# Optimization experiments

Measured on AMD Instinct MI355X. Metric: run time of the kernel, lower is better.

## Reference

```python
import jax, jax.numpy as jnp
import numpy as np

N_BUF = 60000.0
S_INIT = 2.0
S_INV = N_BUF ** S_INIT          # buffer init: N**S_init
S_HAT = (N_BUF ** 2) / S_INV     # == 1.0 at init


def setup_inputs() -> dict:
    key = jax.random.key(0)
    k1, k2 = jax.random.split(key)
    feats = jax.random.normal(k1, (16384, 128), dtype=jnp.float32)
    idx = jax.random.randint(k2, (16384,), 0, 60000).astype(jnp.int64)
    return {"feats": feats, "idx": idx}


def reference(feats, idx):
    # CauchyLoss.forward, faithful to the torch source. Note: the original
    # uses out-of-place masked_fill whose result is discarded, so neither the
    # diagonal nor the positive pairs are zeroed before the row-sum; we
    # replicate that exactly.
    n = feats.shape[0]
    B = n // 2
    sq = jnp.sum(feats * feats, axis=1)                      # [2B]
    d2 = sq[:, None] + sq[None, :] - 2.0 * (feats @ feats.T)  # [2B, 2B]
    d2 = jnp.maximum(d2, 0.0)
    q = 1.0 / (d2 + 1.0)                                      # [2B, 2B]
    # positive pairs: pos_mask = roll(eye(2B), B, dims=1) -> (i, (i+B) % 2B)
    rows = jnp.arange(n)
    qii = q[rows, (rows + B) % n]                             # [2B]
    attractive = -jnp.log(qii)
    repulsive = jnp.log(jnp.sum(q, axis=1)) * S_HAT           # [2B]
    return attractive.mean() + repulsive.mean()
```

## Files before the change

kernel.cpp:

```cpp
#include <hip/hip_runtime.h>
#include <hip/hip_bf16.h>

#define N 16384
#define D 128
#define NTI 128
#define NCHUNK 2112
#define GBLK2 4224
#define B_HALF 8192

typedef __attribute__((ext_vector_type(8))) short short8;
typedef __attribute__((ext_vector_type(4))) float f32x4;

__device__ inline unsigned short f2bf(float x) {
    union { float f; unsigned u; } c; c.f = x;
    unsigned r = c.u + 0x7fffu + ((c.u >> 16) & 1u);
    return (unsigned short)(r >> 16);
}

__global__ __launch_bounds__(256)
void prep_kernel(const float* __restrict__ feats, unsigned short* __restrict__ fbP,
                 float* __restrict__ sq, float* __restrict__ rsum,
                 float* __restrict__ qii) {
    const int g  = blockIdx.x * 256 + threadIdx.x;
    const int p  = g >> 3;
    const int t8 = g & 7;
    const int i0 = p, i1 = p + B_HALF;
    const float4* ra = reinterpret_cast<const float4*>(feats + (size_t)i0 * D + t8 * 16);
    const float4* rb = reinterpret_cast<const float4*>(feats + (size_t)i1 * D + t8 * 16);
    char* da = (char*)fbP + (size_t)(i0 >> 7) * 32768 + (size_t)(i0 & 127) * 16;
    char* db = (char*)fbP + (size_t)(i1 >> 7) * 32768 + (size_t)(i1 & 127) * 16;
    float sa = 0.f, sb = 0.f, dot = 0.f;
#pragma unroll
    for (int c = 0; c < 2; ++c) {
        float4 x0 = ra[2 * c], x1 = ra[2 * c + 1];
        float4 y0 = rb[2 * c], y1 = rb[2 * c + 1];
        sa  += x0.x * x0.x + x0.y * x0.y + x0.z * x0.z + x0.w * x0.w
             + x1.x * x1.x + x1.y * x1.y + x1.z * x1.z + x1.w * x1.w;
        sb  += y0.x * y0.x + y0.y * y0.y + y0.z * y0.z + y0.w * y0.w
             + y1.x * y1.x + y1.y * y1.y + y1.z * y1.z + y1.w * y1.w;
        dot += x0.x * y0.x + x0.y * y0.y + x0.z * y0.z + x0.w * y0.w
             + x1.x * y1.x + x1.y * y1.y + x1.z * y1.z + x1.w * y1.w;
        short8 ca, cb;
        ca[0] = f2bf(x0.x); ca[1] = f2bf(x0.y); ca[2] = f2bf(x0.z); ca[3] = f2bf(x0.w);
        ca[4] = f2bf(x1.x); ca[5] = f2bf(x1.y); ca[6] = f2bf(x1.z); ca[7] = f2bf(x1.w);
        cb[0] = f2bf(y0.x); cb[1] = f2bf(y0.y); cb[2] = f2bf(y0.z); cb[3] = f2bf(y0.w);
        cb[4] = f2bf(y1.x); cb[5] = f2bf(y1.y); cb[6] = f2bf(y1.z); cb[7] = f2bf(y1.w);
        *reinterpret_cast<short8*>(da + (2 * t8 + c) * 2048) = ca;
        *reinterpret_cast<short8*>(db + (2 * t8 + c) * 2048) = cb;
    }
    sa  += __shfl_xor(sa, 1);  sa  += __shfl_xor(sa, 2);  sa  += __shfl_xor(sa, 4);
    sb  += __shfl_xor(sb, 1);  sb  += __shfl_xor(sb, 2);  sb  += __shfl_xor(sb, 4);
    dot += __shfl_xor(dot, 1); dot += __shfl_xor(dot, 2); dot += __shfl_xor(dot, 4);
    if (t8 == 0) {
        sq[i0] = sa; sq[i1] = sb;
        rsum[i0] = 0.f; rsum[i1] = 0.f;
        float d2 = fmaxf(sa + sb - 2.f * dot, 0.f);
        float q = 1.f / (d2 + 1.f);
        qii[i0] = q; qii[i1] = q;
    }
}

__global__ __launch_bounds__(256, 4)
void gram_kernel(const unsigned short* __restrict__ fbP, const float* __restrict__ sq,
                 float* __restrict__ rsum) {
    const int bid  = (blockIdx.x & 7) * (GBLK2 / 8) + (blockIdx.x >> 3);
    const int chnk = bid >> 1;
    const int half = bid & 1;

    int u = (int)((130.0f - sqrtf(16900.0f - 8.0f * (float)chnk)) * 0.25f);
    if (u < 0) u = 0; if (u > 31) u = 31;
    while (u > 0 && 2 * u * (65 - u) > chnk) --u;
    while (2 * (u + 1) * (64 - u) <= chnk) ++u;
    int rem = chnk - 2 * u * (65 - u);
    const int cnt = 32 - u;
    int sub = 0;
    while (rem >= cnt) { rem -= cnt; ++sub; }
    const int ti  = 4 * u + sub;
    const int tj0 = ti + 4 * rem;
    const int nt  = (NTI - tj0 < 4) ? (NTI - tj0) : 4;

    const int tid  = threadIdx.x;
    const int lane = tid & 63;
    const int wid  = tid >> 6;
    const int wr   = wid >> 1;
    const int wc   = wid & 1;
    const int lrow = lane & 15;
    const int lk   = lane >> 4;
    const int row0 = half * 64 + wr * 32;

    const char* pa = (const char*)fbP + (size_t)ti * 32768;
    const int aoff0 = lk * 2048 + (row0 + lrow) * 16;
    const int boff0 = lk * 2048 + (wc * 64 + lrow) * 16;

    float SA[2][4];
#pragma unroll
    for (int m = 0; m < 2; ++m) {
        const float4 v = *reinterpret_cast<const float4*>(
            sq + ti * 128 + row0 + m * 16 + lk * 4);
        SA[m][0] = -0.5f * v.x; SA[m][1] = -0.5f * v.y;
        SA[m][2] = -0.5f * v.z; SA[m][3] = -0.5f * v.w;
    }
    float SB[4][4];
#pragma unroll
    for (int t = 0; t < 4; ++t) {
        const int tt = (tj0 + t < NTI) ? (tj0 + t) : (NTI - 1);
#pragma unroll
        for (int n = 0; n < 4; ++n)
            SB[t][n] = -0.5f * (sq[tt * 128 + wc * 64 + n * 16 + lrow] + 1.0f);
    }

    float racc[2][4];
#pragma unroll
    for (int m = 0; m < 2; ++m)
#pragma unroll
        for (int r = 0; r < 4; ++r) racc[m][r] = 0.f;

#pragma unroll
    for (int t = 0; t < 4; ++t) {
        if (t < nt) {
            const char* pb = (const char*)fbP + (size_t)(tj0 + t) * 32768;

            f32x4 acc[2][4];
#pragma unroll
            for (int m = 0; m < 2; ++m)
#pragma unroll
                for (int n = 0; n < 4; ++n)
#pragma unroll
                    for (int r = 0; r < 4; ++r)
                        acc[m][n][r] = SA[m][r] + SB[t][n];

#pragma unroll
            for (int kk = 0; kk < 4; ++kk) {
                short8 av[2], bv[4];
#pragma unroll
                for (int m = 0; m < 2; ++m)
                    av[m] = *reinterpret_cast<const short8*>(pa + aoff0 + kk * 8192 + m * 256);
#pragma unroll
                for (int n = 0; n < 4; ++n)
                    bv[n] = *reinterpret_cast<const short8*>(pb + boff0 + kk * 8192 + n * 256);
#pragma unroll
                for (int m = 0; m < 2; ++m)
#pragma unroll
                    for (int n = 0; n < 4; ++n)
                        acc[m][n] = __builtin_amdgcn_mfma_f32_16x16x32_bf16(
                            av[m], bv[n], acc[m][n], 0, 0, 0);
            }

            float cloc[4] = {0.f, 0.f, 0.f, 0.f};
#pragma unroll
            for (int m = 0; m < 2; ++m)
#pragma unroll
                for (int n = 0; n < 4; ++n)
#pragma unroll
                    for (int r = 0; r < 4; ++r) {
                        float a = fminf(acc[m][n][r], -0.5f);
                        float q = __builtin_amdgcn_rcpf(a);
                        racc[m][r] += q;
                        cloc[n] += q;
                    }
            if (tj0 + t != ti) {
#pragma unroll
                for (int n = 0; n < 4; ++n) {
                    float v = cloc[n];
                    v += __shfl_xor(v, 16);
                    v += __shfl_xor(v, 32);
                    if (lane < 16)
                        atomicAdd(&rsum[(tj0 + t) * 128 + wc * 64 + n * 16 + lrow],
                                  -0.5f * v);
                }
            }
        }
    }

#pragma unroll
    for (int m = 0; m < 2; ++m)
#pragma unroll
        for (int r = 0; r < 4; ++r) {
            float v = racc[m][r];
            v += __shfl_xor(v, 1);
            v += __shfl_xor(v, 2);
            v += __shfl_xor(v, 4);
            v += __shfl_xor(v, 8);
            if (lrow == 0)
                atomicAdd(&rsum[ti * 128 + row0 + m * 16 + lk * 4 + r], -0.5f * v);
        }
}

__global__ __launch_bounds__(256)
void finish1_kernel(const float* __restrict__ rsum, const float* __restrict__ qii,
                    float* __restrict__ partial) {
    __shared__ float red[4];
    const int i = blockIdx.x * 256 + threadIdx.x;
    float v = __logf(rsum[i]) - __logf(qii[i]);
#pragma unroll
    for (int m = 32; m >= 1; m >>= 1) v += __shfl_xor(v, m);
    if ((threadIdx.x & 63) == 0) red[threadIdx.x >> 6] = v;
    __syncthreads();
    if (threadIdx.x == 0) partial[blockIdx.x] = red[0] + red[1] + red[2] + red[3];
}

__global__ __launch_bounds__(64)
void finish2_kernel(const float* __restrict__ partial, unsigned* __restrict__ out) {
    float v = partial[threadIdx.x];
#pragma unroll
    for (int m = 32; m >= 1; m >>= 1) v += __shfl_xor(v, m);
    if (threadIdx.x == 0) {
        float val = v / (float)N;
        union { float f; unsigned u; } c; c.f = val;
        out[0] = (c.u & 0xFFFF0000u) | (unsigned)f2bf(val);
    }
}

extern "C" void kernel_launch(void* const* d_in, const int* in_sizes, int n_in,
                              void* d_out, int out_size, void* d_ws, size_t ws_size,
                              hipStream_t stream) {
    const float* feats = (const float*)d_in[0];
    char* ws = (char*)d_ws;
    unsigned short* fbP = (unsigned short*)ws;
    float* sq      = (float*)(ws + (size_t)N * D * 2);
    float* rsum    = (float*)(ws + (size_t)N * D * 2 + (size_t)N * 4);
    float* qii     = (float*)(ws + (size_t)N * D * 2 + (size_t)N * 8);
    float* partial = (float*)(ws + (size_t)N * D * 2 + (size_t)N * 12);

    hipLaunchKernelGGL(prep_kernel, dim3(256), dim3(256), 0, stream,
                       feats, fbP, sq, rsum, qii);
    hipLaunchKernelGGL(gram_kernel, dim3(GBLK2), dim3(256), 0, stream,
                       fbP, sq, rsum);
    hipLaunchKernelGGL(finish1_kernel, dim3(64), dim3(256), 0, stream,
                       rsum, qii, partial);
    hipLaunchKernelGGL(finish2_kernel, dim3(1), dim3(64), 0, stream,
                       partial, (unsigned*)d_out);
}
```

Measured before the change: 93.73 us.

## Software-pipeline B-tile loads and hoist A fragments in gram kernel

```diff
diff --git a/kernel.cpp b/kernel.cpp
--- a/kernel.cpp
+++ b/kernel.cpp
@@ -4,7 +4,6 @@
 #define N 16384
 #define D 128
 #define NTI 128
-#define NCHUNK 2112
 #define GBLK2 4224
 #define B_HALF 8192
 
@@ -60,7 +59,7 @@
     }
 }
 
-__global__ __launch_bounds__(256, 4)
+__global__ __launch_bounds__(256, 2)
 void gram_kernel(const unsigned short* __restrict__ fbP, const float* __restrict__ sq,
                  float* __restrict__ rsum) {
     const int bid  = (blockIdx.x & 7) * (GBLK2 / 8) + (blockIdx.x >> 3);
@@ -79,9 +78,8 @@
     const int tj0 = ti + 4 * rem;
     const int nt  = (NTI - tj0 < 4) ? (NTI - tj0) : 4;
 
-    const int tid  = threadIdx.x;
-    const int lane = tid & 63;
-    const int wid  = tid >> 6;
+    const int lane = threadIdx.x & 63;
+    const int wid  = threadIdx.x >> 6;
     const int wr   = wid >> 1;
     const int wc   = wid & 1;
     const int lrow = lane & 15;
@@ -92,6 +90,23 @@
     const int aoff0 = lk * 2048 + (row0 + lrow) * 16;
     const int boff0 = lk * 2048 + (wc * 64 + lrow) * 16;
 
+    const char* pb[4];
+    float w[4];
+#pragma unroll
+    for (int t = 0; t < 4; ++t) {
+        const int tt = tj0 + t;
+        const int tc = (tt < NTI) ? tt : (NTI - 1);
+        pb[t] = (const char*)fbP + (size_t)tc * 32768;
+        w[t]  = (t < nt) ? 1.0f : 0.0f;
+    }
+
+    short8 av[4][2];
+#pragma unroll
+    for (int kk = 0; kk < 4; ++kk)
+#pragma unroll
+        for (int m = 0; m < 2; ++m)
+            av[kk][m] = *reinterpret_cast<const short8*>(pa + aoff0 + kk * 8192 + m * 256);
+
     float SA[2][4];
 #pragma unroll
     for (int m = 0; m < 2; ++m) {
@@ -103,24 +118,43 @@
     float SB[4][4];
 #pragma unroll
     for (int t = 0; t < 4; ++t) {
-        const int tt = (tj0 + t < NTI) ? (tj0 + t) : (NTI - 1);
+        const int tt = tj0 + t;
+        const int tc = (tt < NTI) ? tt : (NTI - 1);
 #pragma unroll
         for (int n = 0; n < 4; ++n)
-            SB[t][n] = -0.5f * (sq[tt * 128 + wc * 64 + n * 16 + lrow] + 1.0f);
+            SB[t][n] = -0.5f * (sq[tc * 128 + wc * 64 + n * 16 + lrow] + 1.0f);
     }
 
     float racc[2][4];
+    float cacc[4][4];
 #pragma unroll
     for (int m = 0; m < 2; ++m)
 #pragma unroll
         for (int r = 0; r < 4; ++r) racc[m][r] = 0.f;
-
-#pragma unroll
-    for (int t = 0; t < 4; ++t) {
-        if (t < nt) {
-            const char* pb = (const char*)fbP + (size_t)(tj0 + t) * 32768;
-
-            f32x4 acc[2][4];
+#pragma unroll
+    for (int t = 0; t < 4; ++t)
+#pragma unroll
+        for (int n = 0; n < 4; ++n) cacc[t][n] = 0.f;
+
+    short8 bs[3][4];
+#define LDB(SET, S)                                                            \
+    {                                                                          \
+        const int t_ = (S) >> 2, k_ = (S) & 3;                                 \
+        _Pragma("unroll")                                                      \
+        for (int n = 0; n < 4; ++n)                                            \
+            bs[SET][n] = *reinterpret_cast<const short8*>(                     \
+                pb[t_] + boff0 + k_ * 8192 + n * 256);                         \
+    }
+
+    LDB(0, 0)
+    LDB(1, 1)
+
+    f32x4 acc[2][4];
+#pragma unroll
+    for (int s = 0; s < 16; ++s) {
+        const int t = s >> 2, kk = s & 3, cur = s % 3, nxt = (s + 2) % 3;
+        if (s + 2 < 16) LDB(nxt, s + 2)
+        if (kk == 0) {
 #pragma unroll
             for (int m = 0; m < 2; ++m)
 #pragma unroll
@@ -128,25 +162,14 @@
 #pragma unroll
                     for (int r = 0; r < 4; ++r)
                         acc[m][n][r] = SA[m][r] + SB[t][n];
-
-#pragma unroll
-            for (int kk = 0; kk < 4; ++kk) {
-                short8 av[2], bv[4];
-#pragma unroll
-                for (int m = 0; m < 2; ++m)
-                    av[m] = *reinterpret_cast<const short8*>(pa + aoff0 + kk * 8192 + m * 256);
-#pragma unroll
-                for (int n = 0; n < 4; ++n)
-                    bv[n] = *reinterpret_cast<const short8*>(pb + boff0 + kk * 8192 + n * 256);
-#pragma unroll
-                for (int m = 0; m < 2; ++m)
-#pragma unroll
-                    for (int n = 0; n < 4; ++n)
-                        acc[m][n] = __builtin_amdgcn_mfma_f32_16x16x32_bf16(
-                            av[m], bv[n], acc[m][n], 0, 0, 0);
-            }
-
-            float cloc[4] = {0.f, 0.f, 0.f, 0.f};
+        }
+#pragma unroll
+        for (int m = 0; m < 2; ++m)
+#pragma unroll
+            for (int n = 0; n < 4; ++n)
+                acc[m][n] = __builtin_amdgcn_mfma_f32_16x16x32_bf16(
+                    av[kk][m], bs[cur][n], acc[m][n], 0, 0, 0);
+        if (kk == 3) {
 #pragma unroll
             for (int m = 0; m < 2; ++m)
 #pragma unroll
@@ -155,22 +178,12 @@
                     for (int r = 0; r < 4; ++r) {
                         float a = fminf(acc[m][n][r], -0.5f);
                         float q = __builtin_amdgcn_rcpf(a);
-                        racc[m][r] += q;
-                        cloc[n] += q;
+                        racc[m][r] = fmaf(w[t], q, racc[m][r]);
+                        cacc[t][n] += q;
                     }
-            if (tj0 + t != ti) {
-#pragma unroll
-                for (int n = 0; n < 4; ++n) {
-                    float v = cloc[n];
-                    v += __shfl_xor(v, 16);
-                    v += __shfl_xor(v, 32);
-                    if (lane < 16)
-                        atomicAdd(&rsum[(tj0 + t) * 128 + wc * 64 + n * 16 + lrow],
-                                  -0.5f * v);
-                }
-            }
-        }
-    }
+        }
+    }
+#undef LDB
 
 #pragma unroll
     for (int m = 0; m < 2; ++m)
@@ -184,6 +197,20 @@
             if (lrow == 0)
                 atomicAdd(&rsum[ti * 128 + row0 + m * 16 + lk * 4 + r], -0.5f * v);
         }
+#pragma unroll
+    for (int t = 0; t < 4; ++t) {
+        if (t < nt && tj0 + t != ti) {
+#pragma unroll
+            for (int n = 0; n < 4; ++n) {
+                float v = cacc[t][n];
+                v += __shfl_xor(v, 16);
+                v += __shfl_xor(v, 32);
+                if (lane < 16)
+                    atomicAdd(&rsum[(tj0 + t) * 128 + wc * 64 + n * 16 + lrow],
+                              -0.5f * v);
+            }
+        }
+    }
 }
 
 __global__ __launch_bounds__(256)
```

Measured after the change: 108.8 us. 16.1% more time.
